# Performance work log

Measured on AMD Instinct MI355X. Metric: run time of the kernel, lower is better.

The kernel has to match this reference:

```python
import jax, jax.numpy as jnp
import numpy as np

B, V = 1, 5
HIMG, WIMG = 512, 640
CF = 32            # feature channels
D = 128            # depth planes
NEAR, FAR = 0.5, 5.0
SCALE = 8          # encoder downsampling (2**3, matches scale_intrinsic s=3)
HF, WF = HIMG // SCALE, WIMG // SCALE


def _conv2d(x, w, b, stride=1):
    y = jax.lax.conv_general_dilated(x, w, (stride, stride), 'SAME', dimension_numbers=('NCHW', 'OIHW', 'NCHW'))
    return y + b[None, :, None, None]


def _conv3d(x, w, b):
    y = jax.lax.conv_general_dilated(x, w, (1, 1, 1), 'SAME', dimension_numbers=('NCDHW', 'OIDHW', 'NCDHW'))
    return y + b[None, :, None, None, None]


def _bilinear(feat, x, y):
    # feat [C,H,W]; x,y [M] pixel coords; zero padding outside image
    C, H, W = feat.shape
    x0 = jnp.floor(x); y0 = jnp.floor(y)
    wx = x - x0; wy = y - y0
    x0i = x0.astype(jnp.int32); y0i = y0.astype(jnp.int32)
    def g(yi, xi):
        inb = ((xi >= 0) & (xi < W) & (yi >= 0) & (yi < H)).astype(feat.dtype)
        v = feat[:, jnp.clip(yi, 0, H - 1), jnp.clip(xi, 0, W - 1)]
        return v * inb
    return (g(y0i, x0i) * (1 - wx) * (1 - wy) + g(y0i, x0i + 1) * wx * (1 - wy)
            + g(y0i + 1, x0i) * (1 - wx) * wy + g(y0i + 1, x0i + 1) * wx * wy)


def _depth_hypotheses():
    # uniform in inverse depth between near and far (inv_depth=True)
    inv = jnp.linspace(1.0 / NEAR, 1.0 / FAR, D, dtype=jnp.float32)
    return 1.0 / inv  # [D]


def _cost_volume(feats, K_feat, poses, depths):
    # feats [V,C,HF,WF], K_feat [3,3], poses [V,4,4] -> variance volume [C,D,HF,WF]
    ys, xs = jnp.meshgrid(jnp.arange(HF, dtype=jnp.float32), jnp.arange(WF, dtype=jnp.float32), indexing='ij')
    pix = jnp.stack([xs.ravel(), ys.ravel(), jnp.ones(HF * WF, jnp.float32)])   # [3,N]
    ray = jnp.linalg.inv(K_feat) @ pix                                          # [3,N]
    pts = (ray[:, None, :] * depths[None, :, None]).reshape(3, -1)              # [3,D*N] ref-cam points
    inv_ref = jnp.linalg.inv(poses[0])
    ref = jnp.broadcast_to(feats[0][:, None], (CF, D, HF, WF))
    s, ss = ref, ref * ref
    for v in range(1, V):
        T = poses[v] @ inv_ref
        Xs = T[:3, :3] @ pts + T[:3, 3:4]
        uvw = K_feat @ Xs
        z = uvw[2]
        valid = (z > 1e-3).astype(jnp.float32)
        zc = jnp.clip(z, 1e-3)
        w = (_bilinear(feats[v], uvw[0] / zc, uvw[1] / zc) * valid).reshape(CF, D, HF, WF)
        s = s + w; ss = ss + w * w
    mean = s / V
    return ss / V - mean * mean


def _resize_bilinear(x, h, w):
    return jax.image.resize(x, (x.shape[0], x.shape[1], h, w), method='bilinear')


def setup_inputs():
    key = jax.random.key(0)
    ks = jax.random.split(key, 12)
    images = jax.random.uniform(ks[0], (B, V, 3, HIMG, WIMG), jnp.float32)
    K = jnp.broadcast_to(jnp.array([[600., 0., 320.], [0., 600., 256.], [0., 0., 1.]], jnp.float32), (B, 3, 3))
    poses = np.zeros((B, V, 4, 4), np.float32)
    for v in range(V):
        a = 0.03 * v
        R = np.array([[np.cos(a), 0, np.sin(a)], [0, 1, 0], [-np.sin(a), 0, np.cos(a)]], np.float32)
        poses[:, v, :3, :3] = R
        poses[:, v, :3, 3] = np.array([-0.08 * v, 0.0, 0.0], np.float32)
        poses[:, v, 3, 3] = 1.0
    poses = jnp.asarray(poses)
    def w(k, shape):
        fan_in = int(np.prod(shape[1:]))
        return jax.random.normal(k, shape, jnp.float32) / np.sqrt(fan_in)
    return dict(
        images=images, K=K, poses=poses,
        enc_w1=w(ks[1], (8, 3, 3, 3)), enc_b1=jnp.zeros(8, jnp.float32),
        enc_w2=w(ks[2], (16, 8, 3, 3)), enc_b2=jnp.zeros(16, jnp.float32),
        enc_w3=w(ks[3], (CF, 16, 3, 3)), enc_b3=jnp.zeros(CF, jnp.float32),
        reg_w1=w(ks[4], (8, CF, 3, 3, 3)), reg_b1=jnp.zeros(8, jnp.float32),
        reg_w2=w(ks[5], (1, 8, 3, 3, 3)), reg_b2=jnp.zeros(1, jnp.float32),
        ref_w1=w(ks[6], (32, 4, 3, 3)), ref_b1=jnp.zeros(32, jnp.float32),
        ref_w2=w(ks[7], (1, 32, 3, 3)), ref_b2=jnp.zeros(1, jnp.float32),
    )


def reference(images, K, poses, enc_w1, enc_b1, enc_w2, enc_b2, enc_w3, enc_b3,
              reg_w1, reg_b1, reg_w2, reg_b2, ref_w1, ref_b1, ref_w2, ref_b2):
    # feature extraction at 1/8 resolution (shared across views)
    x = images.reshape(B * V, 3, HIMG, WIMG)
    x = jax.nn.relu(_conv2d(x, enc_w1, enc_b1, 2))
    x = jax.nn.relu(_conv2d(x, enc_w2, enc_b2, 2))
    feats = _conv2d(x, enc_w3, enc_b3, 2).reshape(B, V, CF, HF, WF)
    K_feat = K.at[:, :2, :].multiply(1.0 / SCALE)   # scale_intrinsic(K, s=3)
    depths = _depth_hypotheses()
    cost = jax.vmap(_cost_volume, in_axes=(0, 0, 0, None))(feats, K_feat, poses, depths)  # [B,CF,D,HF,WF]
    # regularizer -> [B,1,D,HF,WF]
    cost = _conv3d(jax.nn.relu(_conv3d(cost, reg_w1, reg_b1)), reg_w2, reg_b2)
    prob = jax.nn.softmax(cost, axis=2)
    # 4 * avg_pool3d(pad(prob,(0,0,0,0,1,2)),(4,1,1)) == sliding sum of 4 along depth
    pp = jnp.pad(prob, ((0, 0), (0, 0), (1, 2), (0, 0), (0, 0)))
    cs = jnp.concatenate([jnp.zeros_like(pp[:, :, :1]), jnp.cumsum(pp, axis=2)], axis=2)
    sum4 = (cs[:, :, 4:4 + D] - cs[:, :, :D]).squeeze(1)    # [B,D,HF,WF]
    confidence = jnp.max(sum4, axis=1, keepdims=True)        # [B,1,HF,WF]
    regressed = jnp.sum(prob[:, 0] * depths[None, :, None, None], axis=1, keepdims=True)  # [B,1,HF,WF]
    regressed = _resize_bilinear(regressed, HIMG, WIMG)
    confidence = _resize_bilinear(confidence, HIMG, WIMG)
    # refiner: residual depth refinement from [ref_image, depth]
    inp = jnp.concatenate([images[:, 0], regressed], axis=1)
    res = _conv2d(jax.nn.relu(_conv2d(inp, ref_w1, ref_b1)), ref_w2, ref_b2)
    refined = regressed + res
    return confidence, refined
```

## Files before the change

kernel.cpp:

```cpp
#include <hip/hip_runtime.h>
#include <math.h>

#define HIMG 512
#define WIMG 640
#define NPIX (HIMG*WIMG)
#define HF 64
#define WF 80
#define NFP (HF*WF)
#define DH 128
#define CF 32
#define NV 5

#define SZ_X1   (5u*8u*256u*320u)
#define SZ_X2   (5u*16u*128u*160u)
#define SZ_FE   (5u*NFP*CF)
#define SZ_WP   48u
#define SZ_COST ((unsigned)DH*HF*CF*WF)
#define SZ_R1   ((unsigned)DH*HF*8u*WF)
#define SZ_C2   ((unsigned)DH*NFP)

#define OFF_X1   0u
#define OFF_X2   (OFF_X1+SZ_X1)
#define OFF_FE   (OFF_X2+SZ_X2)
#define OFF_WP   (OFF_FE+SZ_FE)
#define OFF_COST (OFF_WP+SZ_WP)
#define OFF_R1   (OFF_COST+SZ_COST)
#define OFF_C2   (OFF_R1+SZ_R1)
#define OFF_RL   (OFF_C2+SZ_C2)
#define OFF_CL   (OFF_RL+NFP)
#define OFF_RU   (OFF_CL+NFP)
#define OFF_WB   (OFF_RU+NPIX)

typedef __attribute__((ext_vector_type(8))) short bf16x8;
typedef __attribute__((ext_vector_type(4))) float f32x4;

__device__ __forceinline__ int iclamp(int v, int lo, int hi){ return v<lo?lo:(v>hi?hi:v); }

__device__ __forceinline__ unsigned short f2bf(float f){
  union { float f; unsigned u; } v; v.f=f;
  unsigned r=v.u+0x7fffu+((v.u>>16)&1u);
  return (unsigned short)(r>>16);
}

__global__ void k_setup(const float* __restrict__ Kin, const float* __restrict__ poses,
                        float* __restrict__ warp) {
  if (threadIdx.x != 0 || blockIdx.x != 0) return;
  float Kf[9];
  for (int i=0;i<9;i++) Kf[i]=Kin[i];
  for (int i=0;i<6;i++) Kf[i]*=0.125f;
  float a=Kf[0],b=Kf[1],c=Kf[2],d=Kf[3],e=Kf[4],f=Kf[5],g=Kf[6],h=Kf[7],ii=Kf[8];
  float det=a*(e*ii-f*h)-b*(d*ii-f*g)+c*(d*h-e*g);
  float id=1.0f/det;
  float Ki[9]={(e*ii-f*h)*id,(c*h-b*ii)*id,(b*f-c*e)*id,
               (f*g-d*ii)*id,(a*ii-c*g)*id,(c*d-a*f)*id,
               (d*h-e*g)*id,(b*g-a*h)*id,(a*e-b*d)*id};
  float R0[9]={poses[0],poses[1],poses[2],poses[4],poses[5],poses[6],poses[8],poses[9],poses[10]};
  float t0[3]={poses[3],poses[7],poses[11]};
  for (int v=1; v<NV; v++) {
    const float* P=poses+16*v;
    float Rv[9]={P[0],P[1],P[2],P[4],P[5],P[6],P[8],P[9],P[10]};
    float tv[3]={P[3],P[7],P[11]};
    float TR[9], Tt[3], M[9], A[9], bb[3];
    for (int r=0;r<3;r++)
      for (int cc=0;cc<3;cc++)
        TR[r*3+cc]=Rv[r*3+0]*R0[cc*3+0]+Rv[r*3+1]*R0[cc*3+1]+Rv[r*3+2]*R0[cc*3+2];
    for (int r=0;r<3;r++)
      Tt[r]=tv[r]-(TR[r*3+0]*t0[0]+TR[r*3+1]*t0[1]+TR[r*3+2]*t0[2]);
    for (int r=0;r<3;r++)
      for (int cc=0;cc<3;cc++)
        M[r*3+cc]=TR[r*3+0]*Ki[0*3+cc]+TR[r*3+1]*Ki[1*3+cc]+TR[r*3+2]*Ki[2*3+cc];
    for (int r=0;r<3;r++)
      for (int cc=0;cc<3;cc++)
        A[r*3+cc]=Kf[r*3+0]*M[0*3+cc]+Kf[r*3+1]*M[1*3+cc]+Kf[r*3+2]*M[2*3+cc];
    for (int r=0;r<3;r++)
      bb[r]=Kf[r*3+0]*Tt[0]+Kf[r*3+1]*Tt[1]+Kf[r*3+2]*Tt[2];
    float* o=warp+(v-1)*12;
    for (int i=0;i<9;i++) o[i]=A[i];
    for (int r=0;r<3;r++) o[9+r]=bb[r];
  }
}

__global__ void k_wprep(const float* __restrict__ w, unsigned short* __restrict__ wb){
  int tid=blockIdx.x*256+threadIdx.x;
  for (int idx=tid; idx<13824; idx+=256){
    int tap=idx>>9; int r=idx&511;
    int lane=r>>3; int j=r&7;
    int n=lane&15; int k=(lane>>4)*8+j;
    int kd=tap/9; int kh=(tap/3)%3; int kw=tap%3;
    float val=(n<8)? w[(((n*32+k)*3+kd)*3+kh)*3+kw] : 0.0f;
    wb[idx]=f2bf(val);
  }
}

__global__ __launch_bounds__(256) void k_conv1(const float* __restrict__ img,
    const float* __restrict__ w, const float* __restrict__ bias, float* __restrict__ x1) {
  __shared__ float wl[216];
  int tid=threadIdx.x;
  for (int i=tid;i<216;i+=256){
    int oc=i&7; int rest=i>>3; int kx=rest%3; int ky=(rest/3)%3; int ic=rest/9;
    wl[i]=w[((oc*3+ic)*3+ky)*3+kx];
  }
  __syncthreads();
  int t=blockIdx.x*256+tid;
  int n=t/81920; int r=t%81920; int oy=r/320; int ox=r%320;
  float acc[8];
  #pragma unroll
  for (int oc=0;oc<8;oc++) acc[oc]=bias[oc];
  for (int ic=0;ic<3;ic++){
    const float* ip = img + (n*3+ic)*NPIX;
    #pragma unroll
    for (int ky=0;ky<3;ky++){
      int iy=2*oy+ky; if (iy>=HIMG) continue;
      #pragma unroll
      for (int kx=0;kx<3;kx++){
        int ix=2*ox+kx; if (ix>=WIMG) continue;
        float v=ip[iy*WIMG+ix];
        const float* ww=&wl[((ic*3+ky)*3+kx)*8];
        #pragma unroll
        for (int oc=0;oc<8;oc++) acc[oc]+=v*ww[oc];
      }
    }
  }
  float* op = x1 + (n*8)*81920 + oy*320+ox;
  #pragma unroll
  for (int oc=0;oc<8;oc++){ float vv=fmaxf(acc[oc],0.0f); op[oc*81920]=vv; }
}

__global__ __launch_bounds__(256) void k_conv2(const float* __restrict__ x1,
    const float* __restrict__ w, const float* __restrict__ bias, float* __restrict__ x2){
  __shared__ float wl[1152];
  int tid=threadIdx.x;
  for (int i=tid;i<1152;i+=256){
    int oc=i&15; int rest=i>>4; int tap=rest%9; int ic=rest/9;
    int ky=tap/3, kx=tap%3;
    wl[i]=w[((oc*8+ic)*3+ky)*3+kx];
  }
  __syncthreads();
  int t=blockIdx.x*256+tid;
  int n=t/20480; int r=t%20480; int oy=r/160; int ox=r%160;
  float acc[16];
  #pragma unroll
  for (int oc=0;oc<16;oc++) acc[oc]=bias[oc];
  for (int ic=0;ic<8;ic++){
    const float* ip=x1+(n*8+ic)*81920;
    #pragma unroll
    for (int ky=0;ky<3;ky++){
      int iy=2*oy+ky; if(iy>=256) continue;
      #pragma unroll
      for (int kx=0;kx<3;kx++){
        int ix=2*ox+kx; if(ix>=320) continue;
        float v=ip[iy*320+ix];
        const float* ww=&wl[(ic*9+ky*3+kx)*16];
        #pragma unroll
        for (int oc=0;oc<16;oc++) acc[oc]+=v*ww[oc];
      }
    }
  }
  float* op=x2+(n*16)*20480+oy*160+ox;
  #pragma unroll
  for (int oc=0;oc<16;oc++){ float vv=fmaxf(acc[oc],0.0f); op[oc*20480]=vv; }
}

__global__ __launch_bounds__(256) void k_conv3(const float* __restrict__ x2,
    const float* __restrict__ w, const float* __restrict__ bias, float* __restrict__ fe){
  __shared__ float wl[4608];
  int tid=threadIdx.x;
  for (int i=tid;i<4608;i+=256){
    int oc=i&31; int rest=i>>5; int tap=rest%9; int ic=rest/9;
    int ky=tap/3,kx=tap%3;
    wl[i]=w[((oc*16+ic)*3+ky)*3+kx];
  }
  __syncthreads();
  int t=blockIdx.x*256+tid;
  int half=t&1; int r=t>>1;
  int n=r/NFP; int p=r%NFP; int oy=p/WF; int ox=p%WF;
  float acc[16];
  #pragma unroll
  for (int oc=0;oc<16;oc++) acc[oc]=bias[half*16+oc];
  for (int ic=0;ic<16;ic++){
    const float* ip=x2+(n*16+ic)*20480;
    #pragma unroll
    for (int ky=0;ky<3;ky++){
      int iy=2*oy+ky; if(iy>=128) continue;
      #pragma unroll
      for (int kx=0;kx<3;kx++){
        int ix=2*ox+kx; if(ix>=160) continue;
        float v=ip[iy*160+ix];
        const float* ww=&wl[(ic*9+ky*3+kx)*32+half*16];
        #pragma unroll
        for (int oc=0;oc<16;oc++) acc[oc]+=v*ww[oc];
      }
    }
  }
  float* op=fe+(size_t)r*CF+half*16;
  #pragma unroll
  for (int q=0;q<4;q++) ((float4*)op)[q]=((float4*)acc)[q];
}

__global__ __launch_bounds__(256) void k_costvol(const float* __restrict__ fe,
    const float* __restrict__ warp, unsigned short* __restrict__ costb){
  __shared__ float pw[80][4][4];
  __shared__ int   po[80][4][4];
  int bid=blockIdx.x;
  int d=bid>>6; int y=bid&63;
  int tid=threadIdx.x;
  float invd=2.0f-(float)d*(1.8f/127.0f);
  float depth=1.0f/invd;
  if (tid<80){
    int x=tid;
    float fx=(float)x, fy=(float)y;
    for (int v=1; v<NV; v++){
      const float* W=warp+(v-1)*12;
      float u_=depth*(W[0]*fx+W[1]*fy+W[2])+W[9];
      float v_=depth*(W[3]*fx+W[4]*fy+W[5])+W[10];
      float z_=depth*(W[6]*fx+W[7]*fy+W[8])+W[11];
      float valid=(z_>0.001f)?1.0f:0.0f;
      float zc=(z_>0.001f)?z_:0.001f;
      float uu=u_/zc, vv=v_/zc;
      float fx0=floorf(uu), fy0=floorf(vv);
      float wx=uu-fx0, wy=vv-fy0;
      int xi=(int)fx0, yi=(int)fy0;
      float m00=((xi>=0)&&(xi<WF)&&(yi>=0)&&(yi<HF))?valid:0.0f;
      float m01=((xi+1>=0)&&(xi+1<WF)&&(yi>=0)&&(yi<HF))?valid:0.0f;
      float m10=((xi>=0)&&(xi<WF)&&(yi+1>=0)&&(yi+1<HF))?valid:0.0f;
      float m11=((xi+1>=0)&&(xi+1<WF)&&(yi+1>=0)&&(yi+1<HF))?valid:0.0f;
      pw[x][v-1][0]=(1.0f-wx)*(1.0f-wy)*m00;
      pw[x][v-1][1]=wx*(1.0f-wy)*m01;
      pw[x][v-1][2]=(1.0f-wx)*wy*m10;
      pw[x][v-1][3]=wx*wy*m11;
      int xc0=iclamp(xi,0,WF-1), xc1=iclamp(xi+1,0,WF-1);
      int yc0=iclamp(yi,0,HF-1), yc1=iclamp(yi+1,0,HF-1);
      po[x][v-1][0]=yc0*WF+xc0;
      po[x][v-1][1]=yc0*WF+xc1;
      po[x][v-1][2]=yc1*WF+xc0;
      po[x][v-1][3]=yc1*WF+xc1;
    }
  }
  __syncthreads();
  int c=tid&31, slot=tid>>5;
  float s[10], ss[10];
  #pragma unroll
  for (int i=0;i<10;i++){
    int px=i*8+slot;
    float r=fe[(size_t)(y*WF+px)*CF+c];
    s[i]=r; ss[i]=r*r;
  }
  for (int v=1; v<NV; v++){
    const float* fb=fe+(size_t)v*NFP*CF;
    #pragma unroll
    for (int i=0;i<10;i++){
      int px=i*8+slot;
      float w0=pw[px][v-1][0], w1=pw[px][v-1][1];
      float w2=pw[px][v-1][2], w3=pw[px][v-1][3];
      int o0=po[px][v-1][0], o1=po[px][v-1][1];
      int o2=po[px][v-1][2], o3=po[px][v-1][3];
      float a=fb[(size_t)o0*CF+c];
      float b=fb[(size_t)o1*CF+c];
      float g=fb[(size_t)o2*CF+c];
      float h=fb[(size_t)o3*CF+c];
      float val=w0*a+w1*b+w2*g+w3*h;
      s[i]+=val; ss[i]+=val*val;
    }
  }
  unsigned short* cp=costb+(size_t)bid*WF*CF;
  #pragma unroll
  for (int i=0;i<10;i++){
    int px=i*8+slot;
    float mean=s[i]*0.2f;
    float var=ss[i]*0.2f-mean*mean;
    cp[(size_t)px*CF+c]=f2bf(var);
  }
}

__global__ __launch_bounds__(256) void k_reg1(const unsigned short* __restrict__ costb,
    const unsigned short* __restrict__ wb, const float* __restrict__ bias, float* __restrict__ r1) {
  int bid=blockIdx.x;
  int sb=(bid&7)*256+(bid>>3);
  int tid=threadIdx.x;
  int row=sb*4+(tid>>6);
  int d=row>>6; int y=row&63;
  int lane=tid&63;
  int m=lane&15, g=lane>>4;
  float binit=(m<8)? bias[m] : 0.0f;
  f32x4 acc[5];
  #pragma unroll
  for (int t=0;t<5;t++) acc[t]={binit,binit,binit,binit};
  for (int kd=0;kd<3;kd++){
    int dd=d-1+kd; if (dd<0||dd>=DH) continue;
    for (int kh=0;kh<3;kh++){
      int yy=y-1+kh; if (yy<0||yy>=HF) continue;
      const unsigned short* rowbase=costb+(size_t)(dd*HF+yy)*WF*CF;
      #pragma unroll
      for (int kw=0;kw<3;kw++){
        int tap=(kd*3+kh)*3+kw;
        bf16x8 bfrag=*(const bf16x8*)(wb+(size_t)tap*512+lane*8);
        #pragma unroll
        for (int t=0;t<5;t++){
          int x=t*16+m+kw-1;
          int xc=iclamp(x,0,WF-1);
          bf16x8 afrag=*(const bf16x8*)(rowbase+(size_t)xc*CF+g*8);
          if (x!=xc){ bf16x8 z={0,0,0,0,0,0,0,0}; afrag=z; }
          acc[t]=__builtin_amdgcn_mfma_f32_16x16x32_bf16(afrag,bfrag,acc[t],0,0,0);
        }
      }
    }
  }
  if (m<8){
    float* op=r1+((size_t)(d*HF+y)*8+m)*WF+g*4;
    #pragma unroll
    for (int t=0;t<5;t++){
      float4 o;
      o.x=fmaxf(acc[t][0],0.0f); o.y=fmaxf(acc[t][1],0.0f);
      o.z=fmaxf(acc[t][2],0.0f); o.w=fmaxf(acc[t][3],0.0f);
      *(float4*)(op+t*16)=o;
    }
  }
}

__global__ __launch_bounds__(256) void k_reg2(const float* __restrict__ r1,
    const float* __restrict__ w, const float* __restrict__ bias, float* __restrict__ c2) {
  __shared__ float wl[216];
  int tid=threadIdx.x;
  for (int i=tid;i<216;i+=256) wl[i]=w[i];
  __syncthreads();
  int bid=blockIdx.x;
  int sb=(bid&7)*160+(bid>>3);
  int t=sb*256+tid;
  int x=t%80; int y=(t/80)&63; int dq=t/5120;
  int d0=dq*2;
  float acc0=bias[0], acc1=bias[0];
  for (int pi=0;pi<4;pi++){
    int dd=d0-1+pi; if (dd<0||dd>=DH) continue;
    bool do0=(pi<3), do1=(pi>0);
    for (int kh=0;kh<3;kh++){
      int yy=y-1+kh; if(yy<0||yy>=HF) continue;
      const float* base=r1+((size_t)(dd*HF+yy)*8)*WF+x;
      #pragma unroll
      for (int c=0;c<8;c++){
        const float* rr=base+(size_t)c*WF;
        float in_[3];
        in_[0]=(x>0)?rr[-1]:0.f; in_[1]=rr[0]; in_[2]=(x<79)?rr[1]:0.f;
        #pragma unroll
        for (int kw=0;kw<3;kw++){
          float v=in_[kw];
          if (do0) acc0+=v*wl[((c*3+pi)*3+kh)*3+kw];
          if (do1) acc1+=v*wl[((c*3+pi-1)*3+kh)*3+kw];
        }
      }
    }
  }
  c2[(size_t)d0*NFP+y*WF+x]=acc0;
  c2[(size_t)(d0+1)*NFP+y*WF+x]=acc1;
}

__global__ __launch_bounds__(256) void k_softmax(const float* __restrict__ c2,
    float* __restrict__ reglow, float* __restrict__ conflow){
  int tid=threadIdx.x;
  int lane=tid&31;
  int p=blockIdx.x*8+(tid>>5);
  const float* cp=c2+p;
  float c[4];
  #pragma unroll
  for (int j=0;j<4;j++) c[j]=cp[(size_t)(lane*4+j)*NFP];
  float m=fmaxf(fmaxf(c[0],c[1]),fmaxf(c[2],c[3]));
  #pragma unroll
  for (int off=1;off<32;off<<=1) m=fmaxf(m,__shfl_xor(m,off));
  float e[4]; float sum=0.f,sumd=0.f;
  #pragma unroll
  for (int j=0;j<4;j++){
    int d=lane*4+j;
    e[j]=expf(c[j]-m);
    sum+=e[j];
    float depth=1.0f/(2.0f-(float)d*(1.8f/127.0f));
    sumd+=e[j]*depth;
  }
  #pragma unroll
  for (int off=1;off<32;off<<=1){ sum+=__shfl_xor(sum,off); sumd+=__shfl_xor(sumd,off); }
  int wl=tid&63;
  float em1=__shfl(e[3],wl-1); if(lane==0) em1=0.f;
  float en0=__shfl(e[0],wl+1); if(lane==31) en0=0.f;
  float en1=__shfl(e[1],wl+1); if(lane==31) en1=0.f;
  float w0=em1 +e[0]+e[1]+e[2];
  float w1=e[0]+e[1]+e[2]+e[3];
  float w2=e[1]+e[2]+e[3]+en0;
  float w3=e[2]+e[3]+en0+en1;
  float mw=fmaxf(fmaxf(w0,w1),fmaxf(w2,w3));
  #pragma unroll
  for (int off=1;off<32;off<<=1) mw=fmaxf(mw,__shfl_xor(mw,off));
  if (lane==0){
    reglow[p]=sumd/sum;
    conflow[p]=mw/sum;
  }
}

__global__ __launch_bounds__(256) void k_upsample(const float* __restrict__ conflow,
    const float* __restrict__ reglow, float* __restrict__ outconf, float* __restrict__ regup){
  int t=blockIdx.x*256+threadIdx.x;
  int plane=t/NPIX; int p=t%NPIX;
  int oy=p/WIMG, ox=p%WIMG;
  float sy=((float)oy+0.5f)*0.125f-0.5f;
  float sx=((float)ox+0.5f)*0.125f-0.5f;
  float fy=floorf(sy), fx=floorf(sx);
  float wy=sy-fy, wx=sx-fx;
  int y0=(int)fy, x0=(int)fx;
  int y0c=iclamp(y0,0,HF-1), y1c=iclamp(y0+1,0,HF-1);
  int x0c=iclamp(x0,0,WF-1), x1c=iclamp(x0+1,0,WF-1);
  const float* s = plane? reglow : conflow;
  float v = s[y0c*WF+x0c]*(1.0f-wx)*(1.0f-wy)+s[y0c*WF+x1c]*wx*(1.0f-wy)
          + s[y1c*WF+x0c]*(1.0f-wx)*wy + s[y1c*WF+x1c]*wx*wy;
  if (plane==0) outconf[p]=v; else regup[p]=v;
}

__global__ __launch_bounds__(256) void k_refine(const float* __restrict__ img,
    const float* __restrict__ regup,
    const float* __restrict__ w1, const float* __restrict__ b1,
    const float* __restrict__ w2, const float* __restrict__ b2,
    float* __restrict__ outref){
  __shared__ __align__(16) float wl1[1152];
  __shared__ float wl2[288];
  __shared__ float bl1[32];
  __shared__ float hid[32*18*20];
  int tid=threadIdx.x;
  for (int i=tid;i<1152;i+=256){
    int oc=i&31; int rest=i>>5; int ic=rest&3; int tap=rest>>2;
    wl1[i]=w1[(oc*4+ic)*9+tap];
  }
  for (int i=tid;i<288;i+=256){
    int ic=i&31; int tap=i>>5;
    wl2[i]=w2[ic*9+tap];
  }
  if (tid<32) bl1[tid]=b1[tid];
  __syncthreads();
  int bx=blockIdx.x, by=blockIdx.y;
  for (int i=tid;i<324;i+=256){
    int hy=i/18, hx=i%18;
    int gy=by*16-1+hy, gx=bx*16-1+hx;
    float a[32];
    if (gy<0||gy>=HIMG||gx<0||gx>=WIMG){
      #pragma unroll
      for (int oc=0;oc<32;oc++) a[oc]=0.0f;
    } else {
      #pragma unroll
      for (int oc=0;oc<32;oc++) a[oc]=bl1[oc];
      #pragma unroll
      for (int ky=0;ky<3;ky++){
        int iy=gy-1+ky; if(iy<0||iy>=HIMG) continue;
        #pragma unroll
        for (int kx=0;kx<3;kx++){
          int ix=gx-1+kx; if(ix<0||ix>=WIMG) continue;
          int tap=ky*3+kx;
          #pragma unroll
          for (int ic=0;ic<4;ic++){
            float v=(ic<3)? img[(size_t)ic*NPIX+(size_t)iy*WIMG+ix]
                          : regup[(size_t)iy*WIMG+ix];
            const float4* wv=(const float4*)&wl1[(tap*4+ic)*32];
            #pragma unroll
            for (int q=0;q<8;q++){
              float4 ww=wv[q];
              a[4*q+0]+=v*ww.x; a[4*q+1]+=v*ww.y;
              a[4*q+2]+=v*ww.z; a[4*q+3]+=v*ww.w;
            }
          }
        }
      }
      #pragma unroll
      for (int oc=0;oc<32;oc++) a[oc]=fmaxf(a[oc],0.0f);
    }
    #pragma unroll
    for (int oc=0;oc<32;oc++) hid[oc*360+hy*20+hx]=a[oc];
  }
  __syncthreads();
  int ty=tid>>4, tx=tid&15;
  float acc=b2[0];
  for (int c=0;c<32;c++){
    const float* hb=&hid[c*360];
    #pragma unroll
    for (int ky=0;ky<3;ky++){
      #pragma unroll
      for (int kx=0;kx<3;kx++){
        acc+=hb[(ty+ky)*20+(tx+kx)]*wl2[(ky*3+kx)*32+c];
      }
    }
  }
  int gy=by*16+ty, gx=bx*16+tx;
  size_t p=(size_t)gy*WIMG+gx;
  outref[p]=regup[p]+acc;
}

extern "C" void kernel_launch(void* const* d_in, const int* in_sizes, int n_in,
                              void* d_out, int out_size, void* d_ws, size_t ws_size,
                              hipStream_t stream) {
  (void)in_sizes; (void)n_in; (void)out_size; (void)ws_size;
  const float* images=(const float*)d_in[0];
  const float* Kmat  =(const float*)d_in[1];
  const float* poses =(const float*)d_in[2];
  const float* enc_w1=(const float*)d_in[3];
  const float* enc_b1=(const float*)d_in[4];
  const float* enc_w2=(const float*)d_in[5];
  const float* enc_b2=(const float*)d_in[6];
  const float* enc_w3=(const float*)d_in[7];
  const float* enc_b3=(const float*)d_in[8];
  const float* reg_w1=(const float*)d_in[9];
  const float* reg_b1=(const float*)d_in[10];
  const float* reg_w2=(const float*)d_in[11];
  const float* reg_b2=(const float*)d_in[12];
  const float* ref_w1=(const float*)d_in[13];
  const float* ref_b1=(const float*)d_in[14];
  const float* ref_w2=(const float*)d_in[15];
  const float* ref_b2=(const float*)d_in[16];
  float* ws=(float*)d_ws;
  float* out=(float*)d_out;

  k_setup<<<1,64,0,stream>>>(Kmat,poses,ws+OFF_WP);
  k_wprep<<<1,256,0,stream>>>(reg_w1,(unsigned short*)(ws+OFF_WB));
  k_conv1<<<1600,256,0,stream>>>(images,enc_w1,enc_b1,ws+OFF_X1);
  k_conv2<<<400,256,0,stream>>>(ws+OFF_X1,enc_w2,enc_b2,ws+OFF_X2);
  k_conv3<<<200,256,0,stream>>>(ws+OFF_X2,enc_w3,enc_b3,ws+OFF_FE);
  k_costvol<<<8192,256,0,stream>>>(ws+OFF_FE,ws+OFF_WP,(unsigned short*)(ws+OFF_COST));
  k_reg1<<<2048,256,0,stream>>>((const unsigned short*)(ws+OFF_COST),
                                (const unsigned short*)(ws+OFF_WB),reg_b1,ws+OFF_R1);
  k_reg2<<<1280,256,0,stream>>>(ws+OFF_R1,reg_w2,reg_b2,ws+OFF_C2);
  k_softmax<<<640,256,0,stream>>>(ws+OFF_C2,ws+OFF_RL,ws+OFF_CL);
  k_upsample<<<2560,256,0,stream>>>(ws+OFF_CL,ws+OFF_RL,out,ws+OFF_RU);
  k_refine<<<dim3(40,32),256,0,stream>>>(images,ws+OFF_RU,ref_w1,ref_b1,ref_w2,ref_b2,out+NPIX);
}
```

Baseline: 463.7 us.

## Stage refine inputs in LDS and compute hidden channels in groups of eight

```diff
diff --git a/kernel.cpp b/kernel.cpp
--- a/kernel.cpp
+++ b/kernel.cpp
@@ -411,74 +411,83 @@
   if (plane==0) outconf[p]=v; else regup[p]=v;
 }
 
-__global__ __launch_bounds__(256) void k_refine(const float* __restrict__ img,
+__global__ __launch_bounds__(256,4) void k_refine(const float* __restrict__ img,
     const float* __restrict__ regup,
     const float* __restrict__ w1, const float* __restrict__ b1,
     const float* __restrict__ w2, const float* __restrict__ b2,
     float* __restrict__ outref){
   __shared__ __align__(16) float wl1[1152];
-  __shared__ float wl2[288];
+  __shared__ __align__(16) float wl2[288];
   __shared__ float bl1[32];
-  __shared__ float hid[32*18*20];
+  __shared__ __align__(16) float in_t[1600];
+  __shared__ __align__(16) float hidc[324*8];
   int tid=threadIdx.x;
   for (int i=tid;i<1152;i+=256){
     int oc=i&31; int rest=i>>5; int ic=rest&3; int tap=rest>>2;
     wl1[i]=w1[(oc*4+ic)*9+tap];
   }
   for (int i=tid;i<288;i+=256){
-    int ic=i&31; int tap=i>>5;
-    wl2[i]=w2[ic*9+tap];
+    int c=i&31; int tap=i>>5;
+    wl2[i]=w2[c*9+tap];
   }
   if (tid<32) bl1[tid]=b1[tid];
-  __syncthreads();
   int bx=blockIdx.x, by=blockIdx.y;
-  for (int i=tid;i<324;i+=256){
-    int hy=i/18, hx=i%18;
-    int gy=by*16-1+hy, gx=bx*16-1+hx;
-    float a[32];
-    if (gy<0||gy>=HIMG||gx<0||gx>=WIMG){
-      #pragma unroll
-      for (int oc=0;oc<32;oc++) a[oc]=0.0f;
-    } else {
-      #pragma unroll
-      for (int oc=0;oc<32;oc++) a[oc]=bl1[oc];
-      #pragma unroll
-      for (int ky=0;ky<3;ky++){
-        int iy=gy-1+ky; if(iy<0||iy>=HIMG) continue;
-        #pragma unroll
-        for (int kx=0;kx<3;kx++){
-          int ix=gx-1+kx; if(ix<0||ix>=WIMG) continue;
-          int tap=ky*3+kx;
+  int gy0=by*16-2, gx0=bx*16-2;
+  for (int i=tid;i<1600;i+=256){
+    int ic=i/400; int r=i%400; int yy=r/20, xx=r%20;
+    int gy=gy0+yy, gx=gx0+xx;
+    float v=0.0f;
+    if (gy>=0 && gy<HIMG && gx>=0 && gx<WIMG)
+      v=(ic<3)? img[(size_t)ic*NPIX+(size_t)gy*WIMG+gx] : regup[(size_t)gy*WIMG+gx];
+    in_t[i]=v;
+  }
+  int ty=tid>>4, tx=tid&15;
+  float acc=b2[0];
+  for (int cg=0; cg<4; ++cg){
+    __syncthreads();
+    for (int px=tid; px<324; px+=256){
+      int hy=px/18, hx=px%18;
+      int ghy=by*16-1+hy, ghx=bx*16-1+hx;
+      float a[8];
+      if (ghy<0||ghy>=HIMG||ghx<0||ghx>=WIMG){
+        #pragma unroll
+        for (int q=0;q<8;q++) a[q]=0.0f;
+      } else {
+        #pragma unroll
+        for (int q=0;q<8;q++) a[q]=bl1[cg*8+q];
+        #pragma unroll
+        for (int ky=0;ky<3;ky++){
           #pragma unroll
-          for (int ic=0;ic<4;ic++){
-            float v=(ic<3)? img[(size_t)ic*NPIX+(size_t)iy*WIMG+ix]
-                          : regup[(size_t)iy*WIMG+ix];
-            const float4* wv=(const float4*)&wl1[(tap*4+ic)*32];
+          for (int kx=0;kx<3;kx++){
+            int tap=ky*3+kx;
+            const float* ip=&in_t[(hy+ky)*20+(hx+kx)];
             #pragma unroll
-            for (int q=0;q<8;q++){
-              float4 ww=wv[q];
-              a[4*q+0]+=v*ww.x; a[4*q+1]+=v*ww.y;
-              a[4*q+2]+=v*ww.z; a[4*q+3]+=v*ww.w;
+            for (int ic=0;ic<4;ic++){
+              float v=ip[ic*400];
+              const float4* wv=(const float4*)&wl1[(tap*4+ic)*32+cg*8];
+              float4 w0=wv[0], w1v=wv[1];
+              a[0]+=v*w0.x; a[1]+=v*w0.y; a[2]+=v*w0.z; a[3]+=v*w0.w;
+              a[4]+=v*w1v.x; a[5]+=v*w1v.y; a[6]+=v*w1v.z; a[7]+=v*w1v.w;
             }
           }
         }
-      }
-      #pragma unroll
-      for (int oc=0;oc<32;oc++) a[oc]=fmaxf(a[oc],0.0f);
-    }
-    #pragma unroll
-    for (int oc=0;oc<32;oc++) hid[oc*360+hy*20+hx]=a[oc];
-  }
-  __syncthreads();
-  int ty=tid>>4, tx=tid&15;
-  float acc=b2[0];
-  for (int c=0;c<32;c++){
-    const float* hb=&hid[c*360];
+        #pragma unroll
+        for (int q=0;q<8;q++) a[q]=fmaxf(a[q],0.0f);
+      }
+      float* hp=&hidc[px*8];
+      ((float4*)hp)[0]=((float4*)a)[0];
+      ((float4*)hp)[1]=((float4*)a)[1];
+    }
+    __syncthreads();
     #pragma unroll
     for (int ky=0;ky<3;ky++){
       #pragma unroll
       for (int kx=0;kx<3;kx++){
-        acc+=hb[(ty+ky)*20+(tx+kx)]*wl2[(ky*3+kx)*32+c];
+        const float* hp=&hidc[((ty+ky)*18+(tx+kx))*8];
+        const float* w8=&wl2[(ky*3+kx)*32+cg*8];
+        float4 h0=((const float4*)hp)[0], h1=((const float4*)hp)[1];
+        acc+=h0.x*w8[0]+h0.y*w8[1]+h0.z*w8[2]+h0.w*w8[3]
+            +h1.x*w8[4]+h1.y*w8[5]+h1.z*w8[6]+h1.w*w8[7];
       }
     }
   }
```

After: 395.5 us. -14.7%, faster.
